# Optimization experiments

Measured on AMD Instinct MI355X. Metric: run time of the kernel, lower is better.

The kernel has to match this reference:

```python
import jax, jax.numpy as jnp
import numpy as np

VIS_DIM, HID_DIM, ATT_DIM = 1024, 512, 256
B, R = 512, 196


def setup_inputs() -> dict:
    key = jax.random.key(0)
    ks = jax.random.split(key, 8)
    s_v = 1.0 / np.sqrt(VIS_DIM)
    s_h = 1.0 / np.sqrt(HID_DIM)
    s_a = 1.0 / np.sqrt(ATT_DIM)
    return {
        "visual_features": jax.random.normal(ks[0], (B, R, VIS_DIM), jnp.float32),
        "hidden_state": jax.random.normal(ks[1], (B, HID_DIM), jnp.float32),
        "Wv": jax.random.uniform(ks[2], (VIS_DIM, ATT_DIM), jnp.float32, -s_v, s_v),
        "bv": jax.random.uniform(ks[3], (ATT_DIM,), jnp.float32, -s_v, s_v),
        "Wh": jax.random.uniform(ks[4], (HID_DIM, ATT_DIM), jnp.float32, -s_h, s_h),
        "bh": jax.random.uniform(ks[5], (ATT_DIM,), jnp.float32, -s_h, s_h),
        "Wa": jax.random.uniform(ks[6], (ATT_DIM,), jnp.float32, -s_a, s_a),
        "ba": jax.random.uniform(ks[7], (), jnp.float32, -s_a, s_a),
    }


def reference(visual_features, hidden_state, Wv, bv, Wh, bh, Wa, ba):
    # visual_features: [B, R, Dv]; hidden_state: [B, Dh]
    v_proj = jnp.einsum('brd,da->bra', visual_features, Wv) + bv   # [B, R, A]
    h_proj = hidden_state @ Wh + bh                                # [B, A]
    joint = jax.nn.relu(v_proj + h_proj[:, None, :])               # [B, R, A]
    scores = jnp.einsum('bra,a->br', joint, Wa) + ba               # [B, R]
    att = jax.nn.softmax(scores, axis=1)                           # softmax over regions
    att_output = jnp.einsum('br,brd->bd', att, visual_features)    # [B, Dv]
    return att_output
```

## Files before the change

### kernel.cpp

```cpp
#include <hip/hip_runtime.h>
#include <hip/hip_bf16.h>
#include <stdint.h>
#include <stddef.h>

#define BATCH 512
#define RSZ   196
#define DV    1024
#define DH    512
#define DA    256

typedef short short8 __attribute__((ext_vector_type(8)));
typedef float f32x4 __attribute__((ext_vector_type(4)));

static __device__ __forceinline__ short f2bf(float f) {
    union { float f; unsigned u; } x; x.f = f;
    unsigned r = x.u + 0x7fffu + ((x.u >> 16) & 1u);
    return (short)(r >> 16);
}

static __device__ __forceinline__ int pk2(float x, float y) {
    float2 f; f.x = x; f.y = y;
    __hip_bfloat162 h = __float22bfloat162_rn(f);
    int r; __builtin_memcpy(&r, &h, 4); return r;
}

static __device__ __forceinline__ void gl_lds16(const short* g, short* s) {
    __builtin_amdgcn_global_load_lds(
        (const __attribute__((address_space(1))) void*)g,
        (__attribute__((address_space(3))) void*)s, 16, 0, 0);
}

__global__ __launch_bounds__(256) void k_prep(const float* __restrict__ Wv,
                                              const float* __restrict__ hs,
                                              const float* __restrict__ Wh,
                                              const float* __restrict__ bh,
                                              const float* __restrict__ bv,
                                              short* __restrict__ WvT,
                                              float* __restrict__ H) {
    int tid = threadIdx.x;
    if (blockIdx.x < 64) {
        __shared__ short tile[16][DA];
        int k0 = blockIdx.x * 16;
#pragma unroll
        for (int r = 0; r < 16; ++r)
            tile[r][tid] = f2bf(Wv[(size_t)(k0 + r) * DA + tid]);
        __syncthreads();
        short o[16];
#pragma unroll
        for (int r = 0; r < 16; ++r) o[r] = tile[r][tid];
        *(short8*)&WvT[(size_t)tid * DV + k0]     = *(short8*)&o[0];
        *(short8*)&WvT[(size_t)tid * DV + k0 + 8] = *(short8*)&o[8];
    } else {
        __shared__ float sh[DH];
        int b = blockIdx.x - 64, a = tid;
        sh[a]       = hs[b * DH + a];
        sh[a + 256] = hs[b * DH + 256 + a];
        __syncthreads();
        float acc = 0.f;
#pragma unroll 8
        for (int k = 0; k < DH; ++k) acc += sh[k] * Wh[k * DA + a];
        H[b * DA + a] = acc + bh[a] + bv[a];
    }
}

#define BK  64
#define LDA 72

__global__ __launch_bounds__(256, 2) void k_fused(const float* __restrict__ vf,
                                                  const short* __restrict__ WvT,
                                                  const float* __restrict__ H,
                                                  const float* __restrict__ Wa,
                                                  const float* __restrict__ ba,
                                                  float* __restrict__ out) {
    __shared__ short As[64 * LDA];
    __shared__ short Bs[DA * BK];
    __shared__ float sH[DA];
    __shared__ float sWa[DA];
    __shared__ float red[64][4];
    __shared__ float sp[64];
    __shared__ float sml[4];

    const int tid = threadIdx.x;
    const int l   = tid & 63;
    const int w   = tid >> 6;
    const int ln  = l & 15;
    const int q   = l >> 4;
    const int b   = blockIdx.x;

    sH[tid]  = H[b * DA + tid];
    sWa[tid] = Wa[tid];
    if (tid == 0) { sml[0] = -1e30f; sml[1] = 0.f; }

    const int ar = tid >> 2;
    const int ac = (tid & 3) * 16;

    const int g   = l >> 3;
    const int c   = l & 7;
    const int csw = c ^ g;
    const short* bsrc = WvT + (size_t)(w * 64 + g) * DV + csw * 8;
    short* bdst = &Bs[(w * 8) * 512];

    float4 O = {0.f, 0.f, 0.f, 0.f};
    const float baS = ba[0];

    __syncthreads();

    for (int t = 0; t < 4; ++t) {
        const int r0    = t * 64;
        const int nrows = (t < 3) ? 64 : (RSZ - 192);
        const int micnt = (t < 3) ? 4 : 1;
        const bool rok  = (ar < nrows);
        const float4* ap = (const float4*)(vf + ((size_t)b * RSZ + r0 + (rok ? ar : 0)) * DV + ac);
        short* awr = &As[ar * LDA + ac];

        f32x4 acc[4][4];
#pragma unroll
        for (int i = 0; i < 4; ++i)
#pragma unroll
            for (int j = 0; j < 4; ++j) acc[i][j] = (f32x4){0.f, 0.f, 0.f, 0.f};

        for (int kt = 0; kt < DV; kt += BK) {
#pragma unroll
            for (int j = 0; j < 8; ++j)
                gl_lds16(bsrc + (size_t)j * 8 * DV + kt, bdst + j * 512);
            int kb = kt >> 2;
            float4 f0, f1, f2, f3;
            if (rok) { f0 = ap[kb]; f1 = ap[kb + 1]; f2 = ap[kb + 2]; f3 = ap[kb + 3]; }
            else     { f0 = f1 = f2 = f3 = (float4){0.f, 0.f, 0.f, 0.f}; }
            union { short8 v; int i[4]; } u0, u1;
            u0.i[0] = pk2(f0.x, f0.y); u0.i[1] = pk2(f0.z, f0.w);
            u0.i[2] = pk2(f1.x, f1.y); u0.i[3] = pk2(f1.z, f1.w);
            u1.i[0] = pk2(f2.x, f2.y); u1.i[1] = pk2(f2.z, f2.w);
            u1.i[2] = pk2(f3.x, f3.y); u1.i[3] = pk2(f3.z, f3.w);
            *(short8*)&awr[0] = u0.v;
            *(short8*)&awr[8] = u1.v;
            __syncthreads();
#pragma unroll
            for (int kk = 0; kk < 2; ++kk) {
                short8 bfr[4];
#pragma unroll
                for (int j = 0; j < 4; ++j) {
                    int n = w * 64 + j * 16 + ln;
                    bfr[j] = *(short8*)&Bs[n * BK + ((4 * kk + q) ^ (ln & 7)) * 8];
                }
#pragma unroll
                for (int i = 0; i < 4; ++i) {
                    if (i < micnt) {
                        short8 afr = *(short8*)&As[(i * 16 + ln) * LDA + kk * 32 + q * 8];
#pragma unroll
                        for (int j = 0; j < 4; ++j)
                            acc[i][j] = __builtin_amdgcn_mfma_f32_16x16x32_bf16(
                                afr, bfr[j], acc[i][j], 0, 0, 0);
                    }
                }
            }
            __syncthreads();
        }

#pragma unroll
        for (int i = 0; i < 4; ++i) {
            if (i < micnt) {
#pragma unroll
                for (int r = 0; r < 4; ++r) {
                    int row = i * 16 + q * 4 + r;
                    float p = 0.f;
#pragma unroll
                    for (int j = 0; j < 4; ++j) {
                        int a   = w * 64 + j * 16 + ln;
                        float v = acc[i][j][r] + sH[a];
                        p += fmaxf(v, 0.f) * sWa[a];
                    }
                    p += __shfl_xor(p, 1);
                    p += __shfl_xor(p, 2);
                    p += __shfl_xor(p, 4);
                    p += __shfl_xor(p, 8);
                    if (ln == 0) red[row][w] = p;
                }
            }
        }
        __syncthreads();

        if (tid < 64) {
            float s = (tid < nrows)
                    ? (red[tid][0] + red[tid][1] + red[tid][2] + red[tid][3] + baS)
                    : -1e30f;
            float tm = s;
#pragma unroll
            for (int mk = 32; mk >= 1; mk >>= 1) tm = fmaxf(tm, __shfl_xor(tm, mk));
            float m_old = sml[0];
            float m_new = fmaxf(m_old, tm);
            float p = (tid < nrows) ? expf(s - m_new) : 0.f;
            sp[tid] = p;
            float ls = p;
#pragma unroll
            for (int mk = 32; mk >= 1; mk >>= 1) ls += __shfl_xor(ls, mk);
            if (tid == 0) {
                float alpha = expf(m_old - m_new);
                sml[2] = alpha;
                sml[1] = sml[1] * alpha + ls;
                sml[0] = m_new;
            }
        }
        __syncthreads();

        float alpha = sml[2];
        O.x *= alpha; O.y *= alpha; O.z *= alpha; O.w *= alpha;
        const float4* vrow = (const float4*)(vf + ((size_t)b * RSZ + r0) * DV) + tid;
        for (int r = 0; r + 3 < nrows; r += 4) {
            float4 v0 = vrow[(r + 0) * (DV / 4)];
            float4 v1 = vrow[(r + 1) * (DV / 4)];
            float4 v2 = vrow[(r + 2) * (DV / 4)];
            float4 v3 = vrow[(r + 3) * (DV / 4)];
            float p0 = sp[r], p1 = sp[r + 1], p2 = sp[r + 2], p3 = sp[r + 3];
            O.x += p0 * v0.x + p1 * v1.x + p2 * v2.x + p3 * v3.x;
            O.y += p0 * v0.y + p1 * v1.y + p2 * v2.y + p3 * v3.y;
            O.z += p0 * v0.z + p1 * v1.z + p2 * v2.z + p3 * v3.z;
            O.w += p0 * v0.w + p1 * v1.w + p2 * v2.w + p3 * v3.w;
        }
    }

    float invl = 1.f / sml[1];
    float4 res = {O.x * invl, O.y * invl, O.z * invl, O.w * invl};
    ((float4*)(out + (size_t)b * DV))[tid] = res;
}

extern "C" void kernel_launch(void* const* d_in, const int* in_sizes, int n_in,
                              void* d_out, int out_size, void* d_ws, size_t ws_size,
                              hipStream_t stream) {
    const float* vf = (const float*)d_in[0];
    const float* hs = (const float*)d_in[1];
    const float* Wv = (const float*)d_in[2];
    const float* bv = (const float*)d_in[3];
    const float* Wh = (const float*)d_in[4];
    const float* bh = (const float*)d_in[5];
    const float* Wa = (const float*)d_in[6];
    const float* ba = (const float*)d_in[7];
    float* out = (float*)d_out;

    char* ws = (char*)d_ws;
    short* WvT = (short*)(ws);
    float* H   = (float*)(ws + (512 << 10));

    k_prep<<<576, 256, 0, stream>>>(Wv, hs, Wh, bh, bv, WvT, H);
    k_fused<<<BATCH, 256, 0, stream>>>(vf, WvT, H, Wa, ba, out);
}
```

Before: 653.8 us.

## Software-pipeline fused attention GEMM with register B operands and overlapped weighted sum

Double-buffers the A tile in LDS and prefetches the next A chunk and the B fragments into registers one step ahead, so global loads overlap the MFMA work. B fragments now come straight from global memory into registers instead of through LDS. The weighted-sum pass for the previous row tile is spread across the next tile's k-loop, and the last four rows are handled after the loop. This raises register pressure and issues more global B loads per wave, which may lower occupancy.

```diff
diff --git a/kernel.cpp b/kernel.cpp
--- a/kernel.cpp
+++ b/kernel.cpp
@@ -22,12 +22,6 @@
     float2 f; f.x = x; f.y = y;
     __hip_bfloat162 h = __float22bfloat162_rn(f);
     int r; __builtin_memcpy(&r, &h, 4); return r;
-}
-
-static __device__ __forceinline__ void gl_lds16(const short* g, short* s) {
-    __builtin_amdgcn_global_load_lds(
-        (const __attribute__((address_space(1))) void*)g,
-        (__attribute__((address_space(3))) void*)s, 16, 0, 0);
 }
 
 __global__ __launch_bounds__(256) void k_prep(const float* __restrict__ Wv,
@@ -66,14 +60,16 @@
 #define BK  64
 #define LDA 72
 
+#define BAR() do { asm volatile("s_waitcnt lgkmcnt(0)" ::: "memory"); \
+                   __builtin_amdgcn_s_barrier(); } while (0)
+
 __global__ __launch_bounds__(256, 2) void k_fused(const float* __restrict__ vf,
                                                   const short* __restrict__ WvT,
                                                   const float* __restrict__ H,
                                                   const float* __restrict__ Wa,
                                                   const float* __restrict__ ba,
                                                   float* __restrict__ out) {
-    __shared__ short As[64 * LDA];
-    __shared__ short Bs[DA * BK];
+    __shared__ short As[2][64 * LDA];
     __shared__ float sH[DA];
     __shared__ float sWa[DA];
     __shared__ float red[64][4];
@@ -93,68 +89,95 @@
 
     const int ar = tid >> 2;
     const int ac = (tid & 3) * 16;
-
-    const int g   = l >> 3;
-    const int c   = l & 7;
-    const int csw = c ^ g;
-    const short* bsrc = WvT + (size_t)(w * 64 + g) * DV + csw * 8;
-    short* bdst = &Bs[(w * 8) * 512];
+    const float* aprow = vf + (size_t)b * RSZ * DV;
+    const short* bp = WvT + (size_t)(w * 64 + ln) * DV + q * 8;
 
     float4 O = {0.f, 0.f, 0.f, 0.f};
     const float baS = ba[0];
 
+    float4 g0, g1, g2, g3;
+    short8 B0[8], B1[8];
+
+    auto issueA = [&](int t, int kt) {
+        int nr = (t < 3) ? 64 : 4;
+        if (ar < nr) {
+            const float4* p4 = (const float4*)(aprow + ((size_t)(t * 64 + ar)) * DV + ac) + (kt >> 2);
+            g0 = p4[0]; g1 = p4[1]; g2 = p4[2]; g3 = p4[3];
+        } else {
+            g0 = g1 = g2 = g3 = (float4){0.f, 0.f, 0.f, 0.f};
+        }
+    };
+    auto loadB = [&](short8 (&Bv)[8], int kt) {
+#pragma unroll
+        for (int j = 0; j < 4; ++j)
+#pragma unroll
+            for (int kk = 0; kk < 2; ++kk)
+                Bv[j * 2 + kk] = *(const short8*)(bp + (size_t)j * 16 * DV + kt + kk * 32);
+    };
+    auto stageA = [&](int buf) {
+        union { short8 v; int i[4]; } u0, u1;
+        u0.i[0] = pk2(g0.x, g0.y); u0.i[1] = pk2(g0.z, g0.w);
+        u0.i[2] = pk2(g1.x, g1.y); u0.i[3] = pk2(g1.z, g1.w);
+        u1.i[0] = pk2(g2.x, g2.y); u1.i[1] = pk2(g2.z, g2.w);
+        u1.i[2] = pk2(g3.x, g3.y); u1.i[3] = pk2(g3.z, g3.w);
+        short* awr = &As[buf][ar * LDA + ac];
+        *(short8*)&awr[0] = u0.v;
+        *(short8*)&awr[8] = u1.v;
+    };
+
+    issueA(0, 0);
+    loadB(B0, 0);
+    stageA(0);
     __syncthreads();
 
     for (int t = 0; t < 4; ++t) {
-        const int r0    = t * 64;
-        const int nrows = (t < 3) ? 64 : (RSZ - 192);
         const int micnt = (t < 3) ? 4 : 1;
-        const bool rok  = (ar < nrows);
-        const float4* ap = (const float4*)(vf + ((size_t)b * RSZ + r0 + (rok ? ar : 0)) * DV + ac);
-        short* awr = &As[ar * LDA + ac];
-
         f32x4 acc[4][4];
 #pragma unroll
         for (int i = 0; i < 4; ++i)
 #pragma unroll
             for (int j = 0; j < 4; ++j) acc[i][j] = (f32x4){0.f, 0.f, 0.f, 0.f};
 
-        for (int kt = 0; kt < DV; kt += BK) {
-#pragma unroll
-            for (int j = 0; j < 8; ++j)
-                gl_lds16(bsrc + (size_t)j * 8 * DV + kt, bdst + j * 512);
-            int kb = kt >> 2;
-            float4 f0, f1, f2, f3;
-            if (rok) { f0 = ap[kb]; f1 = ap[kb + 1]; f2 = ap[kb + 2]; f3 = ap[kb + 3]; }
-            else     { f0 = f1 = f2 = f3 = (float4){0.f, 0.f, 0.f, 0.f}; }
-            union { short8 v; int i[4]; } u0, u1;
-            u0.i[0] = pk2(f0.x, f0.y); u0.i[1] = pk2(f0.z, f0.w);
-            u0.i[2] = pk2(f1.x, f1.y); u0.i[3] = pk2(f1.z, f1.w);
-            u1.i[0] = pk2(f2.x, f2.y); u1.i[1] = pk2(f2.z, f2.w);
-            u1.i[2] = pk2(f3.x, f3.y); u1.i[3] = pk2(f3.z, f3.w);
-            *(short8*)&awr[0] = u0.v;
-            *(short8*)&awr[8] = u1.v;
-            __syncthreads();
+        auto body = [&](int kt, int cur, short8 (&Bc)[8], short8 (&Bn)[8]) {
+            const int  ktn     = kt + BK;
+            const bool tileEnd = (ktn == DV);
+            const int  tn      = tileEnd ? t + 1 : t;
+            const int  kn      = tileEnd ? 0 : ktn;
+            if (tn < 4) { issueA(tn, kn); loadB(Bn, kn); }
+            float4 v0, v1, v2, v3; float p0, p1, p2, p3;
+            const int rb = (kt >> 6) * 4;
+            if (t > 0) {
+                const float4* vp = (const float4*)(aprow + ((size_t)((t - 1) * 64 + rb)) * DV) + tid;
+                v0 = vp[0 * (DV / 4)]; v1 = vp[1 * (DV / 4)];
+                v2 = vp[2 * (DV / 4)]; v3 = vp[3 * (DV / 4)];
+                p0 = sp[rb]; p1 = sp[rb + 1]; p2 = sp[rb + 2]; p3 = sp[rb + 3];
+            }
 #pragma unroll
             for (int kk = 0; kk < 2; ++kk) {
-                short8 bfr[4];
-#pragma unroll
-                for (int j = 0; j < 4; ++j) {
-                    int n = w * 64 + j * 16 + ln;
-                    bfr[j] = *(short8*)&Bs[n * BK + ((4 * kk + q) ^ (ln & 7)) * 8];
-                }
 #pragma unroll
                 for (int i = 0; i < 4; ++i) {
                     if (i < micnt) {
-                        short8 afr = *(short8*)&As[(i * 16 + ln) * LDA + kk * 32 + q * 8];
+                        short8 afr = *(short8*)&As[cur][(i * 16 + ln) * LDA + kk * 32 + q * 8];
 #pragma unroll
                         for (int j = 0; j < 4; ++j)
                             acc[i][j] = __builtin_amdgcn_mfma_f32_16x16x32_bf16(
-                                afr, bfr[j], acc[i][j], 0, 0, 0);
+                                afr, Bc[j * 2 + kk], acc[i][j], 0, 0, 0);
                     }
                 }
             }
-            __syncthreads();
+            if (t > 0) {
+                O.x += p0 * v0.x + p1 * v1.x + p2 * v2.x + p3 * v3.x;
+                O.y += p0 * v0.y + p1 * v1.y + p2 * v2.y + p3 * v3.y;
+                O.z += p0 * v0.z + p1 * v1.z + p2 * v2.z + p3 * v3.z;
+                O.w += p0 * v0.w + p1 * v1.w + p2 * v2.w + p3 * v3.w;
+            }
+            if (tn < 4) stageA(cur ^ 1);
+            BAR();
+        };
+
+        for (int k2 = 0; k2 < DV; k2 += 2 * BK) {
+            body(k2,      0, B0, B1);
+            body(k2 + BK, 1, B1, B0);
         }
 
 #pragma unroll
@@ -180,6 +203,7 @@
         }
         __syncthreads();
 
+        const int nrows = (t < 3) ? 64 : 4;
         if (tid < 64) {
             float s = (tid < nrows)
                     ? (red[tid][0] + red[tid][1] + red[tid][2] + red[tid][3] + baS)
@@ -205,18 +229,17 @@
 
         float alpha = sml[2];
         O.x *= alpha; O.y *= alpha; O.z *= alpha; O.w *= alpha;
-        const float4* vrow = (const float4*)(vf + ((size_t)b * RSZ + r0) * DV) + tid;
-        for (int r = 0; r + 3 < nrows; r += 4) {
-            float4 v0 = vrow[(r + 0) * (DV / 4)];
-            float4 v1 = vrow[(r + 1) * (DV / 4)];
-            float4 v2 = vrow[(r + 2) * (DV / 4)];
-            float4 v3 = vrow[(r + 3) * (DV / 4)];
-            float p0 = sp[r], p1 = sp[r + 1], p2 = sp[r + 2], p3 = sp[r + 3];
-            O.x += p0 * v0.x + p1 * v1.x + p2 * v2.x + p3 * v3.x;
-            O.y += p0 * v0.y + p1 * v1.y + p2 * v2.y + p3 * v3.y;
-            O.z += p0 * v0.z + p1 * v1.z + p2 * v2.z + p3 * v3.z;
-            O.w += p0 * v0.w + p1 * v1.w + p2 * v2.w + p3 * v3.w;
-        }
+    }
+
+    {
+        const float4* vp = (const float4*)(aprow + (size_t)192 * DV) + tid;
+        float4 v0 = vp[0 * (DV / 4)], v1 = vp[1 * (DV / 4)];
+        float4 v2 = vp[2 * (DV / 4)], v3 = vp[3 * (DV / 4)];
+        float p0 = sp[0], p1 = sp[1], p2 = sp[2], p3 = sp[3];
+        O.x += p0 * v0.x + p1 * v1.x + p2 * v2.x + p3 * v3.x;
+        O.y += p0 * v0.y + p1 * v1.y + p2 * v2.y + p3 * v3.y;
+        O.z += p0 * v0.z + p1 * v1.z + p2 * v2.z + p3 * v3.z;
+        O.w += p0 * v0.w + p1 * v1.w + p2 * v2.w + p3 * v3.w;
     }
 
     float invl = 1.f / sml[1];
```

Result: slower. 766.5 us (+17.2%).
